# Kernel optimization log

Hardware: AMD Instinct MI355X
Metric: run time of the kernel (lower is better)

## Reference

```python
import jax, jax.numpy as jnp
import numpy as np

# Winograd F(2,3): m=2 output tile, r=3 filter, alpha=4 input tile, tile stride = 2
M_TILE, R, ALPHA = 2, 3, 4

# input transform (the module's self.B is the standard B^T for F(2,3))
_Bt = jnp.array([[1., 0., -1., 0.],
                 [0., 1.,  1., 0.],
                 [0., -1., 1., 0.],
                 [0., 1.,  0., -1.]], dtype=jnp.float32)
# filter transform G (4x3 standard F(2,3) rows of the module's G)
_G = jnp.array([[1., 0., 0.],
                [0.5, 0.5, 0.5],
                [0.5, -0.5, 0.5],
                [0., 0., 1.]], dtype=jnp.float32)
# inverse (output) transform A^T
_At = jnp.array([[1., 1., 1., 0.],
                 [0., 1., -1., -1.]], dtype=jnp.float32)


def setup_inputs() -> dict:
    key = jax.random.key(0)
    k1, k2, k3 = jax.random.split(key, 3)
    x = jax.random.normal(k1, (32, 128, 64, 64), dtype=jnp.float32)
    weight = jax.random.normal(k2, (256, 128, 3, 3), dtype=jnp.float32) * 0.05
    bias = jax.random.normal(k3, (256,), dtype=jnp.float32) * 0.05
    return {"x": x, "weight": weight, "bias": bias}


def _extract_tiles(x):
    # overlapping alpha x alpha tiles with stride M_TILE: d[b,c,p,q,i,j] = x[b,c,2p+i,2q+j]
    B, C, H, W = x.shape
    th = (H - ALPHA) // M_TILE + 1
    tw = (W - ALPHA) // M_TILE + 1
    rows = (jnp.arange(th) * M_TILE)[:, None, None, None] + jnp.arange(ALPHA)[None, None, :, None]  # (th,1,4,1)
    cols = (jnp.arange(tw) * M_TILE)[None, :, None, None] + jnp.arange(ALPHA)[None, None, None, :]  # (1,tw,1,4)
    return x[:, :, rows, cols]  # (B, C, th, tw, 4, 4)


def _winograd_conv(x, weight, bias):
    B, C, H, W = x.shape
    K = weight.shape[0]
    d = _extract_tiles(x)                                         # (B,C,th,tw,4,4)
    V = jnp.einsum('ai,bcpqij,dj->bcpqad', _Bt, d, _Bt)           # B^T d B
    U = jnp.einsum('ai,kcij,dj->kcad', _G, weight, _G)            # G g G^T, (K,C,4,4)
    M = jnp.einsum('kcad,bcpqad->bkpqad', U, V)                   # elementwise mul + sum over C
    Y = jnp.einsum('ai,bkpqij,dj->bkpqad', _At, M, _At)           # A^T M A, (B,K,th,tw,2,2)
    th, tw = Y.shape[2], Y.shape[3]
    Y = Y.transpose(0, 1, 2, 4, 3, 5).reshape(B, K, th * M_TILE, tw * M_TILE)
    return Y + bias[None, :, None, None]


def reference(x, weight, bias):
    return _winograd_conv(x, weight, bias)
```

## Files before the change

### kernel.cpp

```cpp
#include <hip/hip_runtime.h>

typedef __bf16  bf16x8 __attribute__((ext_vector_type(8)));
typedef float   f32x16 __attribute__((ext_vector_type(16)));

__device__ __forceinline__ unsigned short f2bf(float f) {
    union { float f; unsigned int u; } v; v.f = f;
    unsigned int r = (v.u + 0x7fffu + ((v.u >> 16) & 1u)) >> 16;
    return (unsigned short)r;
}

__device__ __forceinline__ bf16x8 neg8(bf16x8 v) {
    union { bf16x8 b; unsigned u[4]; } t; t.b = v;
    t.u[0] ^= 0x80008000u; t.u[1] ^= 0x80008000u;
    t.u[2] ^= 0x80008000u; t.u[3] ^= 0x80008000u;
    return t.b;
}

__global__ void wino_wtrans(const float* __restrict__ w, unsigned short* __restrict__ Up) {
    int k = blockIdx.x;
    int c = threadIdx.x;
    const float* g = w + (k * 128 + c) * 9;
    float g00=g[0],g01=g[1],g02=g[2],g10=g[3],g11=g[4],g12=g[5],g20=g[6],g21=g[7],g22=g[8];
    float T[4][3];
    T[0][0]=g00;                    T[0][1]=g01;                    T[0][2]=g02;
    T[1][0]=0.5f*(g00+g10+g20);     T[1][1]=0.5f*(g01+g11+g21);     T[1][2]=0.5f*(g02+g12+g22);
    T[2][0]=0.5f*(g00-g10+g20);     T[2][1]=0.5f*(g01-g11+g21);     T[2][2]=0.5f*(g02-g12+g22);
    T[3][0]=g20;                    T[3][1]=g21;                    T[3][2]=g22;
    int cg = c >> 3, j = c & 7;
    #pragma unroll
    for (int a = 0; a < 4; ++a) {
        float u0 = T[a][0];
        float u1 = 0.5f*(T[a][0]+T[a][1]+T[a][2]);
        float u2 = 0.5f*(T[a][0]-T[a][1]+T[a][2]);
        float u3 = T[a][2];
        float uu[4] = {u0,u1,u2,u3};
        #pragma unroll
        for (int d = 0; d < 4; ++d) {
            Up[(((size_t)((a*4+d)*16 + cg))*256 + k)*8 + j] = f2bf(uu[d]);
        }
    }
}

__global__ __launch_bounds__(512, 4) void wino_fused(
        const float* __restrict__ x, const unsigned short* __restrict__ Up,
        const float* __restrict__ bias, float* __restrict__ out)
{
    __shared__ float          Xraw[32*256];
    __shared__ unsigned short Vs[16*2*64*8];

    const bf16x8* U8 = (const bf16x8*)Up;
    const int t  = threadIdx.x;
    const int by = blockIdx.x;
    const int bx = blockIdx.y;

    const int jp   = t & 3;
    const int l4   = (t >> 2) & 15;
    const int qh   = (t >> 6) & 1;
    const int rsel = (t >> 7) & 1;
    const int cgb  = (t >> 8) & 1;
    const int sq   = qh * 16 + l4;
    const int nloc_s = rsel * 32 + sq;
    const bool valid = (sq < 31);

    const int lane = t & 63, wave = t >> 6;
    const int l31 = lane & 31, q2 = lane >> 5;
    const int wn = wave & 1, wk = wave >> 1;
    const int row = bx * 2 + wn;
    const int k0  = by * 128 + wk * 32;
    const int bOff = k0 + l31;
    const int aOff = wn * 32 + l31;

    const float* xg[4];
    #pragma unroll
    for (int bi = 0; bi < 4; ++bi) {
        const int sr  = bi & 1;
        const int srg = bx * 2 + sr;
        const int bg = srg / 31, pg = srg % 31;
        xg[bi] = x + (((size_t)bg * 128) * 64 + 2 * pg + (lane >> 4)) * 64 + (lane & 15) * 4;
    }
    const int clb = wave * 2;

    f32x16 Y00, Y01, Y10, Y11;
    #pragma unroll
    for (int z = 0; z < 16; ++z) { Y00[z]=0.f; Y01[z]=0.f; Y10[z]=0.f; Y11[z]=0.f; }

#define GLOAD(CHK) {                                                           \
    _Pragma("unroll")                                                          \
    for (int bi = 0; bi < 4; ++bi) {                                           \
        const int cl_ = clb + (bi >> 1);                                       \
        const float* gp_ = xg[bi] + (size_t)((CHK)*16 + cl_) * 4096;           \
        __builtin_amdgcn_global_load_lds(                                      \
            (const __attribute__((address_space(1))) void*)gp_,                \
            (__attribute__((address_space(3))) void*)&Xraw[(wave*4 + bi)*256], \
            16, 0, 0);                                                         \
    } }

    GLOAD(0);

    for (int chunk = 0; chunk < 8; ++chunk) {
        asm volatile("s_waitcnt vmcnt(0)" ::: "memory");
        __syncthreads();

        {
            unsigned pk[4][4];
            unsigned* dst = (unsigned*)Vs;
            #pragma unroll
            for (int ch = 0; ch < 2; ++ch) {
                const int g2 = (cgb*8 + jp*2 + ch)*2 + rsel;
                const float* xr = &Xraw[g2*256 + 2*sq];
                float dd[4][4];
                #pragma unroll
                for (int i = 0; i < 4; ++i) {
                    if (valid) {
                        float2 u0 = *(const float2*)(xr + i*64);
                        float2 u1 = *(const float2*)(xr + i*64 + 2);
                        dd[i][0]=u0.x; dd[i][1]=u0.y; dd[i][2]=u1.x; dd[i][3]=u1.y;
                    } else {
                        dd[i][0]=0.f; dd[i][1]=0.f; dd[i][2]=0.f; dd[i][3]=0.f;
                    }
                }
                float s[4][4];
                #pragma unroll
                for (int jj = 0; jj < 4; ++jj) {
                    s[0][jj] = dd[0][jj] - dd[2][jj];
                    s[1][jj] = dd[1][jj] + dd[2][jj];
                    s[2][jj] = dd[2][jj] - dd[1][jj];
                    s[3][jj] = dd[1][jj] - dd[3][jj];
                }
                #pragma unroll
                for (int a = 0; a < 4; ++a) {
                    float v0 = s[a][0] - s[a][2];
                    float v1 = s[a][1] + s[a][2];
                    float v2 = s[a][2] - s[a][1];
                    float v3 = s[a][1] - s[a][3];
                    if (ch == 0) {
                        pk[a][0] = f2bf(v0); pk[a][1] = f2bf(v1);
                        pk[a][2] = f2bf(v2); pk[a][3] = f2bf(v3);
                    } else {
                        pk[a][0] |= (unsigned)f2bf(v0) << 16;
                        pk[a][1] |= (unsigned)f2bf(v1) << 16;
                        pk[a][2] |= (unsigned)f2bf(v2) << 16;
                        pk[a][3] |= (unsigned)f2bf(v3) << 16;
                    }
                }
            }
            const int base = cgb*256 + nloc_s*4 + jp;
            #pragma unroll
            for (int a = 0; a < 4; ++a)
                #pragma unroll
                for (int d = 0; d < 4; ++d)
                    dst[(a*4 + d)*512 + base] = pk[a][d];
        }
        __syncthreads();

        if (chunk < 7) GLOAD(chunk + 1);

        const bf16x8* va = (const bf16x8*)Vs;
        __builtin_amdgcn_s_setprio(1);
        #pragma unroll
        for (int ad = 0; ad < 16; ++ad) {
            const int A_ = ad >> 2, D_ = ad & 3;
            const bool t00 = (A_ <= 2) && (D_ <= 2);
            const bool t01 = (A_ <= 2) && (D_ >= 1);
            const bool t10 = (A_ >= 1) && (D_ <= 2);
            const bool t11 = (A_ >= 1) && (D_ >= 1);
            const bool sd = (D_ >= 2), sa = (A_ >= 2);
            const bool needn = (t01 && sd) || (t10 && sa) || (t11 && (sa != sd));
            bf16x8 av = va[(ad*2 + q2)*64 + aOff];
            bf16x8 bv = U8[(size_t)(ad*16 + chunk*2 + q2)*256 + bOff];
            bf16x8 nv = needn ? neg8(av) : av;
            if (t00) Y00 = __builtin_amdgcn_mfma_f32_32x32x16_bf16(av, bv, Y00, 0, 0, 0);
            if (t01) Y01 = __builtin_amdgcn_mfma_f32_32x32x16_bf16(sd ? nv : av, bv, Y01, 0, 0, 0);
            if (t10) Y10 = __builtin_amdgcn_mfma_f32_32x32x16_bf16(sa ? nv : av, bv, Y10, 0, 0, 0);
            if (t11) Y11 = __builtin_amdgcn_mfma_f32_32x32x16_bf16((sa != sd) ? nv : av, bv, Y11, 0, 0, 0);
        }
        __builtin_amdgcn_s_setprio(0);
    }

    int b = row / 31, p = row % 31;
    int k = k0 + l31;
    float bvs = bias[k];
    float* op = out + (size_t)(b*256 + k) * 62 * 62;
    #pragma unroll
    for (int r = 0; r < 16; ++r) {
        int q = (r & 3) + 8*(r >> 2) + 4*q2;
        if (q < 31) {
            *(float2*)(op + (2*p+0)*62 + 2*q) = make_float2(Y00[r] + bvs, Y01[r] + bvs);
            *(float2*)(op + (2*p+1)*62 + 2*q) = make_float2(Y10[r] + bvs, Y11[r] + bvs);
        }
    }
#undef GLOAD
}

extern "C" void kernel_launch(void* const* d_in, const int* in_sizes, int n_in,
                              void* d_out, int out_size, void* d_ws, size_t ws_size,
                              hipStream_t stream) {
    const float* x    = (const float*)d_in[0];
    const float* w    = (const float*)d_in[1];
    const float* bias = (const float*)d_in[2];
    float* out = (float*)d_out;

    unsigned short* Up = (unsigned short*)d_ws;

    wino_wtrans<<<dim3(256),    dim3(128), 0, stream>>>(w, Up);
    wino_fused <<<dim3(2, 496), dim3(512), 0, stream>>>(x, Up, bias, out);
}
```

Before: 284.7 us.

## Double-buffer LDS and software-pipeline input transform with MFMA phase

Doubles the raw-input and transformed-tile LDS buffers so that each iteration issues the next global load, runs the MFMAs on the previous chunk's transformed tiles, and then transforms the current chunk. This removes one barrier per chunk and lets the VALU transform work overlap with matrix-core work. In exchange, LDS use per block roughly doubles (to about 96KB) and the launch bound drops to 2 blocks per CU, lowering occupancy. The s_setprio hints are also removed.

```diff
diff --git a/kernel.cpp b/kernel.cpp
--- a/kernel.cpp
+++ b/kernel.cpp
@@ -41,12 +41,12 @@
     }
 }
 
-__global__ __launch_bounds__(512, 4) void wino_fused(
+__global__ __launch_bounds__(512, 2) void wino_fused(
         const float* __restrict__ x, const unsigned short* __restrict__ Up,
         const float* __restrict__ bias, float* __restrict__ out)
 {
-    __shared__ float          Xraw[32*256];
-    __shared__ unsigned short Vs[16*2*64*8];
+    __shared__ float          Xraw[2][32*256];
+    __shared__ unsigned short Vs[2][16*2*64*8];
 
     const bf16x8* U8 = (const bf16x8*)Up;
     const int t  = threadIdx.x;
@@ -84,79 +84,20 @@
     #pragma unroll
     for (int z = 0; z < 16; ++z) { Y00[z]=0.f; Y01[z]=0.f; Y10[z]=0.f; Y11[z]=0.f; }
 
-#define GLOAD(CHK) {                                                           \
+#define GLOAD(CHK, BUF) {                                                      \
     _Pragma("unroll")                                                          \
     for (int bi = 0; bi < 4; ++bi) {                                           \
         const int cl_ = clb + (bi >> 1);                                       \
         const float* gp_ = xg[bi] + (size_t)((CHK)*16 + cl_) * 4096;           \
         __builtin_amdgcn_global_load_lds(                                      \
             (const __attribute__((address_space(1))) void*)gp_,                \
-            (__attribute__((address_space(3))) void*)&Xraw[(wave*4 + bi)*256], \
+            (__attribute__((address_space(3))) void*)                          \
+                &Xraw[BUF][(wave*4 + bi)*256],                                 \
             16, 0, 0);                                                         \
     } }
 
-    GLOAD(0);
-
-    for (int chunk = 0; chunk < 8; ++chunk) {
-        asm volatile("s_waitcnt vmcnt(0)" ::: "memory");
-        __syncthreads();
-
-        {
-            unsigned pk[4][4];
-            unsigned* dst = (unsigned*)Vs;
-            #pragma unroll
-            for (int ch = 0; ch < 2; ++ch) {
-                const int g2 = (cgb*8 + jp*2 + ch)*2 + rsel;
-                const float* xr = &Xraw[g2*256 + 2*sq];
-                float dd[4][4];
-                #pragma unroll
-                for (int i = 0; i < 4; ++i) {
-                    if (valid) {
-                        float2 u0 = *(const float2*)(xr + i*64);
-                        float2 u1 = *(const float2*)(xr + i*64 + 2);
-                        dd[i][0]=u0.x; dd[i][1]=u0.y; dd[i][2]=u1.x; dd[i][3]=u1.y;
-                    } else {
-                        dd[i][0]=0.f; dd[i][1]=0.f; dd[i][2]=0.f; dd[i][3]=0.f;
-                    }
-                }
-                float s[4][4];
-                #pragma unroll
-                for (int jj = 0; jj < 4; ++jj) {
-                    s[0][jj] = dd[0][jj] - dd[2][jj];
-                    s[1][jj] = dd[1][jj] + dd[2][jj];
-                    s[2][jj] = dd[2][jj] - dd[1][jj];
-                    s[3][jj] = dd[1][jj] - dd[3][jj];
-                }
-                #pragma unroll
-                for (int a = 0; a < 4; ++a) {
-                    float v0 = s[a][0] - s[a][2];
-                    float v1 = s[a][1] + s[a][2];
-                    float v2 = s[a][2] - s[a][1];
-                    float v3 = s[a][1] - s[a][3];
-                    if (ch == 0) {
-                        pk[a][0] = f2bf(v0); pk[a][1] = f2bf(v1);
-                        pk[a][2] = f2bf(v2); pk[a][3] = f2bf(v3);
-                    } else {
-                        pk[a][0] |= (unsigned)f2bf(v0) << 16;
-                        pk[a][1] |= (unsigned)f2bf(v1) << 16;
-                        pk[a][2] |= (unsigned)f2bf(v2) << 16;
-                        pk[a][3] |= (unsigned)f2bf(v3) << 16;
-                    }
-                }
-            }
-            const int base = cgb*256 + nloc_s*4 + jp;
-            #pragma unroll
-            for (int a = 0; a < 4; ++a)
-                #pragma unroll
-                for (int d = 0; d < 4; ++d)
-                    dst[(a*4 + d)*512 + base] = pk[a][d];
-        }
-        __syncthreads();
-
-        if (chunk < 7) GLOAD(chunk + 1);
-
-        const bf16x8* va = (const bf16x8*)Vs;
-        __builtin_amdgcn_s_setprio(1);
+    auto mfma_phase = [&](int mk) {
+        const bf16x8* va = (const bf16x8*)Vs[mk & 1];
         #pragma unroll
         for (int ad = 0; ad < 16; ++ad) {
             const int A_ = ad >> 2, D_ = ad & 3;
@@ -167,15 +108,78 @@
             const bool sd = (D_ >= 2), sa = (A_ >= 2);
             const bool needn = (t01 && sd) || (t10 && sa) || (t11 && (sa != sd));
             bf16x8 av = va[(ad*2 + q2)*64 + aOff];
-            bf16x8 bv = U8[(size_t)(ad*16 + chunk*2 + q2)*256 + bOff];
+            bf16x8 bv = U8[(size_t)(ad*16 + mk*2 + q2)*256 + bOff];
             bf16x8 nv = needn ? neg8(av) : av;
             if (t00) Y00 = __builtin_amdgcn_mfma_f32_32x32x16_bf16(av, bv, Y00, 0, 0, 0);
             if (t01) Y01 = __builtin_amdgcn_mfma_f32_32x32x16_bf16(sd ? nv : av, bv, Y01, 0, 0, 0);
             if (t10) Y10 = __builtin_amdgcn_mfma_f32_32x32x16_bf16(sa ? nv : av, bv, Y10, 0, 0, 0);
             if (t11) Y11 = __builtin_amdgcn_mfma_f32_32x32x16_bf16((sa != sd) ? nv : av, bv, Y11, 0, 0, 0);
         }
-        __builtin_amdgcn_s_setprio(0);
-    }
+    };
+
+    auto t_phase = [&](int ck) {
+        unsigned pk[4][4];
+        unsigned* dst = (unsigned*)Vs[ck & 1];
+        const float* xbuf = Xraw[ck & 1];
+        #pragma unroll
+        for (int ch = 0; ch < 2; ++ch) {
+            const int g2 = (cgb*8 + jp*2 + ch)*2 + rsel;
+            const float* xr = &xbuf[g2*256 + 2*sq];
+            float dd[4][4];
+            #pragma unroll
+            for (int i = 0; i < 4; ++i) {
+                if (valid) {
+                    float2 u0 = *(const float2*)(xr + i*64);
+                    float2 u1 = *(const float2*)(xr + i*64 + 2);
+                    dd[i][0]=u0.x; dd[i][1]=u0.y; dd[i][2]=u1.x; dd[i][3]=u1.y;
+                } else {
+                    dd[i][0]=0.f; dd[i][1]=0.f; dd[i][2]=0.f; dd[i][3]=0.f;
+                }
+            }
+            float s[4][4];
+            #pragma unroll
+            for (int jj = 0; jj < 4; ++jj) {
+                s[0][jj] = dd[0][jj] - dd[2][jj];
+                s[1][jj] = dd[1][jj] + dd[2][jj];
+                s[2][jj] = dd[2][jj] - dd[1][jj];
+                s[3][jj] = dd[1][jj] - dd[3][jj];
+            }
+            #pragma unroll
+            for (int a = 0; a < 4; ++a) {
+                float v0 = s[a][0] - s[a][2];
+                float v1 = s[a][1] + s[a][2];
+                float v2 = s[a][2] - s[a][1];
+                float v3 = s[a][1] - s[a][3];
+                if (ch == 0) {
+                    pk[a][0] = f2bf(v0); pk[a][1] = f2bf(v1);
+                    pk[a][2] = f2bf(v2); pk[a][3] = f2bf(v3);
+                } else {
+                    pk[a][0] |= (unsigned)f2bf(v0) << 16;
+                    pk[a][1] |= (unsigned)f2bf(v1) << 16;
+                    pk[a][2] |= (unsigned)f2bf(v2) << 16;
+                    pk[a][3] |= (unsigned)f2bf(v3) << 16;
+                }
+            }
+        }
+        const int base = cgb*256 + nloc_s*4 + jp;
+        #pragma unroll
+        for (int a = 0; a < 4; ++a)
+            #pragma unroll
+            for (int d = 0; d < 4; ++d)
+                dst[(a*4 + d)*512 + base] = pk[a][d];
+    };
+
+    GLOAD(0, 0);
+
+    for (int chunk = 0; chunk < 8; ++chunk) {
+        asm volatile("s_waitcnt vmcnt(0)" ::: "memory");
+        __syncthreads();
+        if (chunk < 7) GLOAD(chunk + 1, (chunk + 1) & 1);
+        if (chunk > 0) mfma_phase(chunk - 1);
+        t_phase(chunk);
+    }
+    __syncthreads();
+    mfma_phase(7);
 
     int b = row / 31, p = row % 31;
     int k = k0 + l31;
```

Result: slower. 293.0 us (+2.9%).
